# Kernel tuning notes

Measured on AMD Instinct MI355X. Metric: run time of the kernel, lower is better.

Reference implementation:

```python
import jax, jax.numpy as jnp
import numpy as np

N_FEATURE = 12
SIGMA = 0.015
NODES = jnp.linspace(0.0, 0.3, 12)  # RBF centers, matches torch.linspace(0,0.3,12)

B, N, K, FIN = 16, 4096, 32, 4


def setup_inputs() -> dict:
    key = jax.random.key(0)
    ks = jax.random.split(key, 24)

    def make_d(ki, kd):
        idx = jax.random.randint(ki, (B, N, K), 0, N).astype(jnp.float32)
        dist = jax.random.uniform(kd, (B, N, K), minval=0.0, maxval=0.3)
        return jnp.stack([idx, dist], axis=-1)  # [B,N,K,2]

    def lin(kw, kb, fin, fout):
        W = jax.random.normal(kw, (fin, fout), jnp.float32) * (1.0 / np.sqrt(fin))
        b = jax.random.normal(kb, (fout,), jnp.float32) * 0.01
        return W, b

    x = jax.random.normal(ks[0], (B, N, FIN), jnp.float32)
    d1 = make_d(ks[1], ks[2])
    d0 = make_d(ks[3], ks[4])
    dm1 = make_d(ks[5], ks[6])
    mask = jnp.ones((B, N), dtype=bool)

    We, be = lin(ks[7], ks[8], FIN, N_FEATURE)
    Wm1, bm1 = lin(ks[9], ks[10], N_FEATURE + 12, N_FEATURE)
    Wu1, bu1 = lin(ks[11], ks[12], 2 * N_FEATURE, N_FEATURE)
    Wm0, bm0 = lin(ks[13], ks[14], N_FEATURE + 12, N_FEATURE)
    Wu0, bu0 = lin(ks[15], ks[16], 2 * N_FEATURE, N_FEATURE)
    Wmm1, bmm1 = lin(ks[17], ks[18], N_FEATURE + 12, N_FEATURE)
    Wum1, bum1 = lin(ks[19], ks[20], 2 * N_FEATURE, N_FEATURE)

    return {"x": x, "d1": d1, "d0": d0, "dm1": dm1, "mask": mask,
            "We": We, "be": be, "Wm1": Wm1, "bm1": bm1, "Wu1": Wu1, "bu1": bu1,
            "Wm0": Wm0, "bm0": bm0, "Wu0": Wu0, "bu0": bu0,
            "Wmm1": Wmm1, "bmm1": bmm1, "Wum1": Wum1, "bum1": bum1}


def _branch(h, d, Wm, bm, Wu, bu):
    # d: [B,N,K,2] -> channel 0 neighbor index, channel 1 distance
    idx = d[..., 0].astype(jnp.int32)                     # [B,N,K]
    rbf = jnp.exp(-((d[..., 1][..., None] - NODES) ** 2) / (2.0 * SIGMA ** 2))  # [B,N,K,12]
    hj = jax.vmap(lambda hb, ib: hb[ib])(h, idx)          # gather: [B,N,K,F]
    hd = jnp.concatenate([hj, rbf], axis=-1)              # [B,N,K,F+12]
    m = jax.nn.relu(hd @ Wm + bm).sum(axis=2)             # [B,N,F]
    return jax.nn.sigmoid(jnp.concatenate([h, m], axis=-1) @ Wu + bu)  # [B,N,F]


def reference(x, d1, d0, dm1, mask,
              We, be, Wm1, bm1, Wu1, bu1,
              Wm0, bm0, Wu0, bu0,
              Wmm1, bmm1, Wum1, bum1):
    h = jax.nn.relu(x @ We + be)                          # [B,N,12]
    h1 = _branch(h, d1, Wm1, bm1, Wu1, bu1)
    h0 = _branch(h, d0, Wm0, bm0, Wu0, bu0)
    hm1 = _branch(h, dm1, Wmm1, bmm1, Wum1, bum1)
    return (h1, h0, hm1)
```

## Files before the change

kernel.cpp:

```cpp
#include <hip/hip_runtime.h>
#include <hip/hip_fp16.h>
#include <math.h>

#define BBAT 16
#define NNODE 4096
#define KNB 32
#define NF 12
#define TBL 512
#define NPB 820
#define TMAIN 832

#define LDS_BYTES 110616

__device__ __forceinline__ __half2 u2h(unsigned int u) { __half2 h; __builtin_memcpy(&h, &u, 4); return h; }
__device__ __forceinline__ unsigned int h2u(__half2 h) { unsigned int u; __builtin_memcpy(&u, &h, 4); return u; }
__device__ __forceinline__ float4 ldf4(const float* p) { return *(const float4*)p; }

__global__ __launch_bounds__(256) void prep_kernel(
    const float* __restrict__ x, const float* __restrict__ We, const float* __restrict__ be,
    const float* __restrict__ Wm1, const float* __restrict__ bm1,
    const float* __restrict__ Wm0, const float* __restrict__ bm0,
    const float* __restrict__ Wmm1, const float* __restrict__ bmm1,
    float* __restrict__ h, uint4* __restrict__ gA, uint2* __restrict__ gB)
{
    const int node = blockIdx.x * 256 + threadIdx.x;
    float4 xv = ((const float4*)x)[node];
    float hv[NF];
#pragma unroll
    for (int f = 0; f < NF; f++) {
        float s = be[f];
        s = fmaf(xv.x, We[0 * NF + f], s);
        s = fmaf(xv.y, We[1 * NF + f], s);
        s = fmaf(xv.z, We[2 * NF + f], s);
        s = fmaf(xv.w, We[3 * NF + f], s);
        hv[f] = fmaxf(s, 0.0f);
    }
    float4* hp = (float4*)(h + (size_t)node * NF);
    hp[0] = make_float4(hv[0], hv[1], hv[2], hv[3]);
    hp[1] = make_float4(hv[4], hv[5], hv[6], hv[7]);
    hp[2] = make_float4(hv[8], hv[9], hv[10], hv[11]);

#define DO_G(BR, WM, BM) {                                                     \
        float g[NF];                                                           \
        _Pragma("unroll") for (int c = 0; c < NF; c++) {                       \
            float s = BM[c];                                                   \
            _Pragma("unroll") for (int j = 0; j < NF; j++)                     \
                s = fmaf(hv[j], WM[j * NF + c], s);                            \
            g[c] = s;                                                          \
        }                                                                      \
        uint4 a; uint2 bv;                                                     \
        a.x  = h2u(__floats2half2_rn(g[0],  g[1]));                            \
        a.y  = h2u(__floats2half2_rn(g[2],  g[3]));                            \
        a.z  = h2u(__floats2half2_rn(g[4],  g[5]));                            \
        a.w  = h2u(__floats2half2_rn(g[6],  g[7]));                            \
        bv.x = h2u(__floats2half2_rn(g[8],  g[9]));                            \
        bv.y = h2u(__floats2half2_rn(g[10], g[11]));                           \
        gA[(size_t)(BR) * 65536 + node] = a;                                   \
        gB[(size_t)(BR) * 65536 + node] = bv;                                  \
    }
    DO_G(0, Wm1, bm1)
    DO_G(1, Wm0, bm0)
    DO_G(2, Wmm1, bmm1)
#undef DO_G
}

__global__ __launch_bounds__(256) void table_kernel(
    const float* __restrict__ Wm1, const float* __restrict__ Wm0, const float* __restrict__ Wmm1,
    uint4* __restrict__ tA, uint2* __restrict__ tB)
{
    const int br = blockIdx.x;
    const float* Wm = (br == 0) ? Wm1 : (br == 1) ? Wm0 : Wmm1;
    for (int e = threadIdx.x; e < TBL + 1; e += 256) {
        float dd = (float)e * (0.3f / (float)TBL);
        float rbf[12];
#pragma unroll
        for (int j = 0; j < 12; j++) {
            float t = dd - (0.3f / 11.0f) * (float)j;
            rbf[j] = expf(-2222.2222222222f * t * t);
        }
        float ph[NF];
#pragma unroll
        for (int c = 0; c < NF; c++) {
            float s = 0.0f;
#pragma unroll
            for (int j = 0; j < 12; j++) s = fmaf(rbf[j], Wm[(12 + j) * NF + c], s);
            ph[c] = s;
        }
        uint4 a; uint2 bv;
        a.x  = h2u(__floats2half2_rn(ph[0],  ph[1]));
        a.y  = h2u(__floats2half2_rn(ph[2],  ph[3]));
        a.z  = h2u(__floats2half2_rn(ph[4],  ph[5]));
        a.w  = h2u(__floats2half2_rn(ph[6],  ph[7]));
        bv.x = h2u(__floats2half2_rn(ph[8],  ph[9]));
        bv.y = h2u(__floats2half2_rn(ph[10], ph[11]));
        tA[br * (TBL + 1) + e] = a;
        tB[br * (TBL + 1) + e] = bv;
    }
}

__global__ __launch_bounds__(TMAIN) void main_kernel(
    const float* __restrict__ h,
    const uint4* __restrict__ gA, const uint2* __restrict__ gB,
    const uint4* __restrict__ tA, const uint2* __restrict__ tB,
    const float* __restrict__ d1, const float* __restrict__ d0, const float* __restrict__ dm1,
    const float* __restrict__ Wu1, const float* __restrict__ bu1,
    const float* __restrict__ Wu0, const float* __restrict__ bu0,
    const float* __restrict__ Wum1, const float* __restrict__ bum1,
    float* __restrict__ out)
{
    extern __shared__ char smem[];
    uint4* gAl = (uint4*)smem;
    uint2* gBl = (uint2*)(smem + 65536);
    uint4* tAl = (uint4*)(smem + 98304);
    uint2* tBl = (uint2*)(smem + 106512);

    const int q = blockIdx.x, b = blockIdx.y, br = blockIdx.z;
    const int tid = threadIdx.x;
    const size_t slice = (size_t)(br * BBAT + b) * NNODE;

    {
        const uint4* gAg = gA + slice;
        const uint2* gBg = gB + slice;
        for (int i = tid; i < NNODE; i += TMAIN) { gAl[i] = gAg[i]; gBl[i] = gBg[i]; }
        const uint4* tAg = tA + br * (TBL + 1);
        const uint2* tBg = tB + br * (TBL + 1);
        for (int i = tid; i < TBL + 1; i += TMAIN) { tAl[i] = tAg[i]; tBl[i] = tBg[i]; }
    }
    __syncthreads();

    const int n = q * NPB + tid;
    if (tid >= NPB || n >= NNODE) return;

    const float* dsel = (br == 0) ? d1 : (br == 1) ? d0 : dm1;
    const float* Wu   = (br == 0) ? Wu1 : (br == 1) ? Wu0 : Wum1;
    const float* bu   = (br == 0) ? bu1 : (br == 1) ? bu0 : bum1;

    float m[NF];
#pragma unroll
    for (int f = 0; f < NF; f++) m[f] = 0.0f;

    const float4* dp = (const float4*)(dsel + ((size_t)b * NNODE + n) * (size_t)(KNB * 2));

#define ACC(O, G, T0, T1) {                                                    \
        __half2 t0 = u2h(T0), t1 = u2h(T1);                                    \
        __half2 phi = __hfma2(f2, __hsub2(t1, t0), t0);                        \
        __half2 s2 = __hadd2(u2h(G), phi);                                     \
        float2 sf = __half22float2(s2);                                        \
        m[O]     += fmaxf(sf.x, 0.0f);                                         \
        m[O + 1] += fmaxf(sf.y, 0.0f);                                         \
    }

#pragma unroll
    for (int kt = 0; kt < 4; kt++) {
        float4 e0 = dp[kt * 4 + 0];
        float4 e1 = dp[kt * 4 + 1];
        float4 e2 = dp[kt * 4 + 2];
        float4 e3 = dp[kt * 4 + 3];
        float idxf[8] = { e0.x, e0.z, e1.x, e1.z, e2.x, e2.z, e3.x, e3.z };
        float dist[8] = { e0.y, e0.w, e1.y, e1.w, e2.y, e2.w, e3.y, e3.w };
#pragma unroll
        for (int ee = 0; ee < 8; ee++) {
            int j = (int)idxf[ee];
            uint4 ga = gAl[j];
            uint2 gb = gBl[j];
            float uu = dist[ee] * ((float)TBL / 0.3f);
            int i = (int)uu;
            i = min(i, TBL - 1);
            float fr = uu - (float)i;
            __half2 f2 = __float2half2_rn(fr);
            uint4 a0 = tAl[i];
            uint2 b0 = tBl[i];
            uint4 a1 = tAl[i + 1];
            uint2 b1 = tBl[i + 1];
            ACC(0,  ga.x, a0.x, a1.x)
            ACC(2,  ga.y, a0.y, a1.y)
            ACC(4,  ga.z, a0.z, a1.z)
            ACC(6,  ga.w, a0.w, a1.w)
            ACC(8,  gb.x, b0.x, b1.x)
            ACC(10, gb.y, b0.y, b1.y)
        }
    }
#undef ACC

    const float* hp = h + ((size_t)b * NNODE + n) * NF;
    float4 h0 = ldf4(hp), h1v = ldf4(hp + 4), h2v = ldf4(hp + 8);
    float hv[NF] = { h0.x, h0.y, h0.z, h0.w, h1v.x, h1v.y, h1v.z, h1v.w,
                     h2v.x, h2v.y, h2v.z, h2v.w };
    float ov[NF];
#pragma unroll
    for (int f = 0; f < NF; f++) {
        float a = bu[f];
#pragma unroll
        for (int j = 0; j < NF; j++) a = fmaf(hv[j], Wu[j * NF + f], a);
#pragma unroll
        for (int j = 0; j < NF; j++) a = fmaf(m[j], Wu[(NF + j) * NF + f], a);
        ov[f] = 1.0f / (1.0f + __expf(-a));
    }
    float* op = out + (slice + n) * NF;
    ((float4*)op)[0] = make_float4(ov[0], ov[1], ov[2],  ov[3]);
    ((float4*)op)[1] = make_float4(ov[4], ov[5], ov[6],  ov[7]);
    ((float4*)op)[2] = make_float4(ov[8], ov[9], ov[10], ov[11]);
}

extern "C" void kernel_launch(void* const* d_in, const int* in_sizes, int n_in,
                              void* d_out, int out_size, void* d_ws, size_t ws_size,
                              hipStream_t stream)
{
    const float* x    = (const float*)d_in[0];
    const float* d1   = (const float*)d_in[1];
    const float* d0   = (const float*)d_in[2];
    const float* dm1  = (const float*)d_in[3];
    const float* We   = (const float*)d_in[5];
    const float* be   = (const float*)d_in[6];
    const float* Wm1  = (const float*)d_in[7];
    const float* bm1  = (const float*)d_in[8];
    const float* Wu1  = (const float*)d_in[9];
    const float* bu1  = (const float*)d_in[10];
    const float* Wm0  = (const float*)d_in[11];
    const float* bm0  = (const float*)d_in[12];
    const float* Wu0  = (const float*)d_in[13];
    const float* bu0  = (const float*)d_in[14];
    const float* Wmm1 = (const float*)d_in[15];
    const float* bmm1 = (const float*)d_in[16];
    const float* Wum1 = (const float*)d_in[17];
    const float* bum1 = (const float*)d_in[18];

    char* ws = (char*)d_ws;
    float* h  = (float*)ws;
    uint4* gA = (uint4*)(ws + 3145728);
    uint2* gB = (uint2*)(ws + 6291456);
    uint4* tA = (uint4*)(ws + 7864320);
    uint2* tB = (uint2*)(ws + 7888944);

    hipFuncSetAttribute((const void*)main_kernel,
                        hipFuncAttributeMaxDynamicSharedMemorySize, LDS_BYTES);

    prep_kernel<<<dim3(256), 256, 0, stream>>>(
        x, We, be, Wm1, bm1, Wm0, bm0, Wmm1, bmm1, h, gA, gB);
    table_kernel<<<dim3(3), 256, 0, stream>>>(Wm1, Wm0, Wmm1, tA, tB);
    main_kernel<<<dim3(5, BBAT, 3), TMAIN, LDS_BYTES, stream>>>(
        h, gA, gB, tA, tB, d1, d0, dm1,
        Wu1, bu1, Wu0, bu0, Wum1, bum1, (float*)d_out);
}
```

Before: 149.0 us.

## Fuse prep and table kernels into main kernel, computing gathers and table in LDS

```diff
diff --git a/kernel.cpp b/kernel.cpp
--- a/kernel.cpp
+++ b/kernel.cpp
@@ -16,92 +16,11 @@
 __device__ __forceinline__ unsigned int h2u(__half2 h) { unsigned int u; __builtin_memcpy(&u, &h, 4); return u; }
 __device__ __forceinline__ float4 ldf4(const float* p) { return *(const float4*)p; }
 
-__global__ __launch_bounds__(256) void prep_kernel(
+__global__ __launch_bounds__(TMAIN) void fused_kernel(
     const float* __restrict__ x, const float* __restrict__ We, const float* __restrict__ be,
     const float* __restrict__ Wm1, const float* __restrict__ bm1,
     const float* __restrict__ Wm0, const float* __restrict__ bm0,
     const float* __restrict__ Wmm1, const float* __restrict__ bmm1,
-    float* __restrict__ h, uint4* __restrict__ gA, uint2* __restrict__ gB)
-{
-    const int node = blockIdx.x * 256 + threadIdx.x;
-    float4 xv = ((const float4*)x)[node];
-    float hv[NF];
-#pragma unroll
-    for (int f = 0; f < NF; f++) {
-        float s = be[f];
-        s = fmaf(xv.x, We[0 * NF + f], s);
-        s = fmaf(xv.y, We[1 * NF + f], s);
-        s = fmaf(xv.z, We[2 * NF + f], s);
-        s = fmaf(xv.w, We[3 * NF + f], s);
-        hv[f] = fmaxf(s, 0.0f);
-    }
-    float4* hp = (float4*)(h + (size_t)node * NF);
-    hp[0] = make_float4(hv[0], hv[1], hv[2], hv[3]);
-    hp[1] = make_float4(hv[4], hv[5], hv[6], hv[7]);
-    hp[2] = make_float4(hv[8], hv[9], hv[10], hv[11]);
-
-#define DO_G(BR, WM, BM) {                                                     \
-        float g[NF];                                                           \
-        _Pragma("unroll") for (int c = 0; c < NF; c++) {                       \
-            float s = BM[c];                                                   \
-            _Pragma("unroll") for (int j = 0; j < NF; j++)                     \
-                s = fmaf(hv[j], WM[j * NF + c], s);                            \
-            g[c] = s;                                                          \
-        }                                                                      \
-        uint4 a; uint2 bv;                                                     \
-        a.x  = h2u(__floats2half2_rn(g[0],  g[1]));                            \
-        a.y  = h2u(__floats2half2_rn(g[2],  g[3]));                            \
-        a.z  = h2u(__floats2half2_rn(g[4],  g[5]));                            \
-        a.w  = h2u(__floats2half2_rn(g[6],  g[7]));                            \
-        bv.x = h2u(__floats2half2_rn(g[8],  g[9]));                            \
-        bv.y = h2u(__floats2half2_rn(g[10], g[11]));                           \
-        gA[(size_t)(BR) * 65536 + node] = a;                                   \
-        gB[(size_t)(BR) * 65536 + node] = bv;                                  \
-    }
-    DO_G(0, Wm1, bm1)
-    DO_G(1, Wm0, bm0)
-    DO_G(2, Wmm1, bmm1)
-#undef DO_G
-}
-
-__global__ __launch_bounds__(256) void table_kernel(
-    const float* __restrict__ Wm1, const float* __restrict__ Wm0, const float* __restrict__ Wmm1,
-    uint4* __restrict__ tA, uint2* __restrict__ tB)
-{
-    const int br = blockIdx.x;
-    const float* Wm = (br == 0) ? Wm1 : (br == 1) ? Wm0 : Wmm1;
-    for (int e = threadIdx.x; e < TBL + 1; e += 256) {
-        float dd = (float)e * (0.3f / (float)TBL);
-        float rbf[12];
-#pragma unroll
-        for (int j = 0; j < 12; j++) {
-            float t = dd - (0.3f / 11.0f) * (float)j;
-            rbf[j] = expf(-2222.2222222222f * t * t);
-        }
-        float ph[NF];
-#pragma unroll
-        for (int c = 0; c < NF; c++) {
-            float s = 0.0f;
-#pragma unroll
-            for (int j = 0; j < 12; j++) s = fmaf(rbf[j], Wm[(12 + j) * NF + c], s);
-            ph[c] = s;
-        }
-        uint4 a; uint2 bv;
-        a.x  = h2u(__floats2half2_rn(ph[0],  ph[1]));
-        a.y  = h2u(__floats2half2_rn(ph[2],  ph[3]));
-        a.z  = h2u(__floats2half2_rn(ph[4],  ph[5]));
-        a.w  = h2u(__floats2half2_rn(ph[6],  ph[7]));
-        bv.x = h2u(__floats2half2_rn(ph[8],  ph[9]));
-        bv.y = h2u(__floats2half2_rn(ph[10], ph[11]));
-        tA[br * (TBL + 1) + e] = a;
-        tB[br * (TBL + 1) + e] = bv;
-    }
-}
-
-__global__ __launch_bounds__(TMAIN) void main_kernel(
-    const float* __restrict__ h,
-    const uint4* __restrict__ gA, const uint2* __restrict__ gB,
-    const uint4* __restrict__ tA, const uint2* __restrict__ tB,
     const float* __restrict__ d1, const float* __restrict__ d0, const float* __restrict__ dm1,
     const float* __restrict__ Wu1, const float* __restrict__ bu1,
     const float* __restrict__ Wu0, const float* __restrict__ bu0,
@@ -118,13 +37,65 @@
     const int tid = threadIdx.x;
     const size_t slice = (size_t)(br * BBAT + b) * NNODE;
 
-    {
-        const uint4* gAg = gA + slice;
-        const uint2* gBg = gB + slice;
-        for (int i = tid; i < NNODE; i += TMAIN) { gAl[i] = gAg[i]; gBl[i] = gBg[i]; }
-        const uint4* tAg = tA + br * (TBL + 1);
-        const uint2* tBg = tB + br * (TBL + 1);
-        for (int i = tid; i < TBL + 1; i += TMAIN) { tAl[i] = tAg[i]; tBl[i] = tBg[i]; }
+    const float* Wm = (br == 0) ? Wm1 : (br == 1) ? Wm0 : Wmm1;
+    const float* bm = (br == 0) ? bm1 : (br == 1) ? bm0 : bmm1;
+
+    if (tid <= TBL) {
+        float dd = (float)tid * (0.3f / (float)TBL);
+        float rbf[12];
+#pragma unroll
+        for (int j = 0; j < 12; j++) {
+            float t = dd - (0.3f / 11.0f) * (float)j;
+            rbf[j] = expf(-2222.2222222222f * t * t);
+        }
+        float ph[NF];
+#pragma unroll
+        for (int c = 0; c < NF; c++) {
+            float s = 0.0f;
+#pragma unroll
+            for (int j = 0; j < 12; j++) s = fmaf(rbf[j], Wm[(12 + j) * NF + c], s);
+            ph[c] = s;
+        }
+        uint4 a; uint2 bv;
+        a.x  = h2u(__floats2half2_rn(ph[0],  ph[1]));
+        a.y  = h2u(__floats2half2_rn(ph[2],  ph[3]));
+        a.z  = h2u(__floats2half2_rn(ph[4],  ph[5]));
+        a.w  = h2u(__floats2half2_rn(ph[6],  ph[7]));
+        bv.x = h2u(__floats2half2_rn(ph[8],  ph[9]));
+        bv.y = h2u(__floats2half2_rn(ph[10], ph[11]));
+        tAl[tid] = a;
+        tBl[tid] = bv;
+    }
+
+    for (int i = tid; i < NNODE; i += TMAIN) {
+        float4 xv = ((const float4*)x)[(size_t)b * NNODE + i];
+        float hv[NF];
+#pragma unroll
+        for (int f = 0; f < NF; f++) {
+            float s = be[f];
+            s = fmaf(xv.x, We[0 * NF + f], s);
+            s = fmaf(xv.y, We[1 * NF + f], s);
+            s = fmaf(xv.z, We[2 * NF + f], s);
+            s = fmaf(xv.w, We[3 * NF + f], s);
+            hv[f] = fmaxf(s, 0.0f);
+        }
+        float g[NF];
+#pragma unroll
+        for (int c = 0; c < NF; c++) {
+            float s = bm[c];
+#pragma unroll
+            for (int j = 0; j < NF; j++) s = fmaf(hv[j], Wm[j * NF + c], s);
+            g[c] = s;
+        }
+        uint4 a; uint2 bv;
+        a.x  = h2u(__floats2half2_rn(g[0],  g[1]));
+        a.y  = h2u(__floats2half2_rn(g[2],  g[3]));
+        a.z  = h2u(__floats2half2_rn(g[4],  g[5]));
+        a.w  = h2u(__floats2half2_rn(g[6],  g[7]));
+        bv.x = h2u(__floats2half2_rn(g[8],  g[9]));
+        bv.y = h2u(__floats2half2_rn(g[10], g[11]));
+        gAl[i] = a;
+        gBl[i] = bv;
     }
     __syncthreads();
 
@@ -182,10 +153,18 @@
     }
 #undef ACC
 
-    const float* hp = h + ((size_t)b * NNODE + n) * NF;
-    float4 h0 = ldf4(hp), h1v = ldf4(hp + 4), h2v = ldf4(hp + 8);
-    float hv[NF] = { h0.x, h0.y, h0.z, h0.w, h1v.x, h1v.y, h1v.z, h1v.w,
-                     h2v.x, h2v.y, h2v.z, h2v.w };
+    float4 xv = ((const float4*)x)[(size_t)b * NNODE + n];
+    float hv[NF];
+#pragma unroll
+    for (int f = 0; f < NF; f++) {
+        float s = be[f];
+        s = fmaf(xv.x, We[0 * NF + f], s);
+        s = fmaf(xv.y, We[1 * NF + f], s);
+        s = fmaf(xv.z, We[2 * NF + f], s);
+        s = fmaf(xv.w, We[3 * NF + f], s);
+        hv[f] = fmaxf(s, 0.0f);
+    }
+
     float ov[NF];
 #pragma unroll
     for (int f = 0; f < NF; f++) {
@@ -225,20 +204,10 @@
     const float* Wum1 = (const float*)d_in[17];
     const float* bum1 = (const float*)d_in[18];
 
-    char* ws = (char*)d_ws;
-    float* h  = (float*)ws;
-    uint4* gA = (uint4*)(ws + 3145728);
-    uint2* gB = (uint2*)(ws + 6291456);
-    uint4* tA = (uint4*)(ws + 7864320);
-    uint2* tB = (uint2*)(ws + 7888944);
-
-    hipFuncSetAttribute((const void*)main_kernel,
+    hipFuncSetAttribute((const void*)fused_kernel,
                         hipFuncAttributeMaxDynamicSharedMemorySize, LDS_BYTES);
 
-    prep_kernel<<<dim3(256), 256, 0, stream>>>(
-        x, We, be, Wm1, bm1, Wm0, bm0, Wmm1, bmm1, h, gA, gB);
-    table_kernel<<<dim3(3), 256, 0, stream>>>(Wm1, Wm0, Wmm1, tA, tB);
-    main_kernel<<<dim3(5, BBAT, 3), TMAIN, LDS_BYTES, stream>>>(
-        h, gA, gB, tA, tB, d1, d0, dm1,
-        Wu1, bu1, Wu0, bu0, Wum1, bum1, (float*)d_out);
+    fused_kernel<<<dim3(5, BBAT, 3), TMAIN, LDS_BYTES, stream>>>(
+        x, We, be, Wm1, bm1, Wm0, bm0, Wmm1, bmm1,
+        d1, d0, dm1, Wu1, bu1, Wu0, bu0, Wum1, bum1, (float*)d_out);
 }
```

Result: no change. 150.9 us (+1.3%).

## Restructure main kernel: global gathers, two threads per node, XCD-aware block mapping

Applied to the files above, without the earlier changes.

```diff
diff --git a/kernel.cpp b/kernel.cpp
--- a/kernel.cpp
+++ b/kernel.cpp
@@ -7,21 +7,46 @@
 #define KNB 32
 #define NF 12
 #define TBL 512
-#define NPB 820
-#define TMAIN 832
-
-#define LDS_BYTES 110616
+#define TMAIN 512
+#define NPB 256
 
 __device__ __forceinline__ __half2 u2h(unsigned int u) { __half2 h; __builtin_memcpy(&h, &u, 4); return h; }
 __device__ __forceinline__ unsigned int h2u(__half2 h) { unsigned int u; __builtin_memcpy(&u, &h, 4); return u; }
-__device__ __forceinline__ float4 ldf4(const float* p) { return *(const float4*)p; }
+
+__device__ __forceinline__ void phi_entry(int e, const float* __restrict__ Wm, float* ph)
+{
+    float dd = (float)e * (0.3f / (float)TBL);
+    float rbf[12];
+#pragma unroll
+    for (int j = 0; j < 12; j++) {
+        float t = dd - (0.3f / 11.0f) * (float)j;
+        rbf[j] = expf(-2222.2222222222f * t * t);
+    }
+#pragma unroll
+    for (int c = 0; c < NF; c++) {
+        float s = 0.0f;
+#pragma unroll
+        for (int j = 0; j < 12; j++) s = fmaf(rbf[j], Wm[(12 + j) * NF + c], s);
+        ph[c] = s;
+    }
+}
+
+__device__ __forceinline__ void pack12(const float* v, uint4& a, uint2& bv)
+{
+    a.x  = h2u(__floats2half2_rn(v[0],  v[1]));
+    a.y  = h2u(__floats2half2_rn(v[2],  v[3]));
+    a.z  = h2u(__floats2half2_rn(v[4],  v[5]));
+    a.w  = h2u(__floats2half2_rn(v[6],  v[7]));
+    bv.x = h2u(__floats2half2_rn(v[8],  v[9]));
+    bv.y = h2u(__floats2half2_rn(v[10], v[11]));
+}
 
 __global__ __launch_bounds__(256) void prep_kernel(
     const float* __restrict__ x, const float* __restrict__ We, const float* __restrict__ be,
     const float* __restrict__ Wm1, const float* __restrict__ bm1,
     const float* __restrict__ Wm0, const float* __restrict__ bm0,
     const float* __restrict__ Wmm1, const float* __restrict__ bmm1,
-    float* __restrict__ h, uint4* __restrict__ gA, uint2* __restrict__ gB)
+    uint4* __restrict__ gA, uint2* __restrict__ gB, uint4* __restrict__ tP)
 {
     const int node = blockIdx.x * 256 + threadIdx.x;
     float4 xv = ((const float4*)x)[node];
@@ -35,10 +60,6 @@
         s = fmaf(xv.w, We[3 * NF + f], s);
         hv[f] = fmaxf(s, 0.0f);
     }
-    float4* hp = (float4*)(h + (size_t)node * NF);
-    hp[0] = make_float4(hv[0], hv[1], hv[2], hv[3]);
-    hp[1] = make_float4(hv[4], hv[5], hv[6], hv[7]);
-    hp[2] = make_float4(hv[8], hv[9], hv[10], hv[11]);
 
 #define DO_G(BR, WM, BM) {                                                     \
         float g[NF];                                                           \
@@ -49,12 +70,7 @@
             g[c] = s;                                                          \
         }                                                                      \
         uint4 a; uint2 bv;                                                     \
-        a.x  = h2u(__floats2half2_rn(g[0],  g[1]));                            \
-        a.y  = h2u(__floats2half2_rn(g[2],  g[3]));                            \
-        a.z  = h2u(__floats2half2_rn(g[4],  g[5]));                            \
-        a.w  = h2u(__floats2half2_rn(g[6],  g[7]));                            \
-        bv.x = h2u(__floats2half2_rn(g[8],  g[9]));                            \
-        bv.y = h2u(__floats2half2_rn(g[10], g[11]));                           \
+        pack12(g, a, bv);                                                      \
         gA[(size_t)(BR) * 65536 + node] = a;                                   \
         gB[(size_t)(BR) * 65536 + node] = bv;                                  \
     }
@@ -62,84 +78,68 @@
     DO_G(1, Wm0, bm0)
     DO_G(2, Wmm1, bmm1)
 #undef DO_G
-}
-
-__global__ __launch_bounds__(256) void table_kernel(
-    const float* __restrict__ Wm1, const float* __restrict__ Wm0, const float* __restrict__ Wmm1,
-    uint4* __restrict__ tA, uint2* __restrict__ tB)
-{
-    const int br = blockIdx.x;
-    const float* Wm = (br == 0) ? Wm1 : (br == 1) ? Wm0 : Wmm1;
-    for (int e = threadIdx.x; e < TBL + 1; e += 256) {
-        float dd = (float)e * (0.3f / (float)TBL);
-        float rbf[12];
-#pragma unroll
-        for (int j = 0; j < 12; j++) {
-            float t = dd - (0.3f / 11.0f) * (float)j;
-            rbf[j] = expf(-2222.2222222222f * t * t);
+
+    if (blockIdx.x < 3) {
+        const int br = blockIdx.x;
+        const float* Wm = (br == 0) ? Wm1 : (br == 1) ? Wm0 : Wmm1;
+        for (int i = threadIdx.x; i < TBL; i += 256) {
+            float p0[NF], p1[NF];
+            phi_entry(i, Wm, p0);
+            phi_entry(i + 1, Wm, p1);
+            uint4 a0, a1; uint2 b0, b1;
+            pack12(p0, a0, b0);
+            pack12(p1, a1, b1);
+            uint4 w0 = make_uint4(a0.x, a0.y, a0.z, a0.w);
+            uint4 w1 = make_uint4(b0.x, b0.y, a1.x, a1.y);
+            uint4 w2 = make_uint4(a1.z, a1.w, b1.x, b1.y);
+            uint4* dst = tP + ((size_t)br * TBL + i) * 3;
+            dst[0] = w0; dst[1] = w1; dst[2] = w2;
         }
-        float ph[NF];
-#pragma unroll
-        for (int c = 0; c < NF; c++) {
-            float s = 0.0f;
-#pragma unroll
-            for (int j = 0; j < 12; j++) s = fmaf(rbf[j], Wm[(12 + j) * NF + c], s);
-            ph[c] = s;
-        }
-        uint4 a; uint2 bv;
-        a.x  = h2u(__floats2half2_rn(ph[0],  ph[1]));
-        a.y  = h2u(__floats2half2_rn(ph[2],  ph[3]));
-        a.z  = h2u(__floats2half2_rn(ph[4],  ph[5]));
-        a.w  = h2u(__floats2half2_rn(ph[6],  ph[7]));
-        bv.x = h2u(__floats2half2_rn(ph[8],  ph[9]));
-        bv.y = h2u(__floats2half2_rn(ph[10], ph[11]));
-        tA[br * (TBL + 1) + e] = a;
-        tB[br * (TBL + 1) + e] = bv;
-    }
-}
-
-__global__ __launch_bounds__(TMAIN) void main_kernel(
-    const float* __restrict__ h,
-    const uint4* __restrict__ gA, const uint2* __restrict__ gB,
-    const uint4* __restrict__ tA, const uint2* __restrict__ tB,
+    }
+}
+
+__global__ __launch_bounds__(TMAIN, 6) void main_kernel(
+    const float* __restrict__ x, const float* __restrict__ We, const float* __restrict__ be,
+    const uint4* __restrict__ gA, const uint2* __restrict__ gB, const uint4* __restrict__ tP,
     const float* __restrict__ d1, const float* __restrict__ d0, const float* __restrict__ dm1,
     const float* __restrict__ Wu1, const float* __restrict__ bu1,
     const float* __restrict__ Wu0, const float* __restrict__ bu0,
     const float* __restrict__ Wum1, const float* __restrict__ bum1,
     float* __restrict__ out)
 {
-    extern __shared__ char smem[];
-    uint4* gAl = (uint4*)smem;
-    uint2* gBl = (uint2*)(smem + 65536);
-    uint4* tAl = (uint4*)(smem + 98304);
-    uint2* tBl = (uint2*)(smem + 106512);
-
-    const int q = blockIdx.x, b = blockIdx.y, br = blockIdx.z;
+    __shared__ uint4 tPl[TBL * 3];
+
+    const int w = blockIdx.x;
+    const int xcd = w & 7;
+    const int k = w >> 3;
+    const int slice = xcd + 8 * (k >> 4);
+    const int chunk = k & 15;
+    const int br = slice / BBAT;
+    const int b  = slice % BBAT;
+
     const int tid = threadIdx.x;
-    const size_t slice = (size_t)(br * BBAT + b) * NNODE;
 
     {
-        const uint4* gAg = gA + slice;
-        const uint2* gBg = gB + slice;
-        for (int i = tid; i < NNODE; i += TMAIN) { gAl[i] = gAg[i]; gBl[i] = gBg[i]; }
-        const uint4* tAg = tA + br * (TBL + 1);
-        const uint2* tBg = tB + br * (TBL + 1);
-        for (int i = tid; i < TBL + 1; i += TMAIN) { tAl[i] = tAg[i]; tBl[i] = tBg[i]; }
+        const uint4* tPg = tP + (size_t)br * TBL * 3;
+        for (int i = tid; i < TBL * 3; i += TMAIN) tPl[i] = tPg[i];
     }
     __syncthreads();
 
-    const int n = q * NPB + tid;
-    if (tid >= NPB || n >= NNODE) return;
+    const int nl = tid >> 1, half = tid & 1;
+    const int n = chunk * NPB + nl;
 
     const float* dsel = (br == 0) ? d1 : (br == 1) ? d0 : dm1;
     const float* Wu   = (br == 0) ? Wu1 : (br == 1) ? Wu0 : Wum1;
     const float* bu   = (br == 0) ? bu1 : (br == 1) ? bu0 : bum1;
 
+    const uint4* gAg = gA + (size_t)slice * NNODE;
+    const uint2* gBg = gB + (size_t)slice * NNODE;
+
     float m[NF];
 #pragma unroll
     for (int f = 0; f < NF; f++) m[f] = 0.0f;
 
-    const float4* dp = (const float4*)(dsel + ((size_t)b * NNODE + n) * (size_t)(KNB * 2));
+    const float4* dp = (const float4*)(dsel + ((size_t)b * NNODE + n) * (size_t)(KNB * 2)) + half * 8;
 
 #define ACC(O, G, T0, T1) {                                                    \
         __half2 t0 = u2h(T0), t1 = u2h(T1);                                    \
@@ -151,7 +151,7 @@
     }
 
 #pragma unroll
-    for (int kt = 0; kt < 4; kt++) {
+    for (int kt = 0; kt < 2; kt++) {
         float4 e0 = dp[kt * 4 + 0];
         float4 e1 = dp[kt * 4 + 1];
         float4 e2 = dp[kt * 4 + 2];
@@ -161,45 +161,58 @@
 #pragma unroll
         for (int ee = 0; ee < 8; ee++) {
             int j = (int)idxf[ee];
-            uint4 ga = gAl[j];
-            uint2 gb = gBl[j];
+            uint4 ga = gAg[j];
+            uint2 gb = gBg[j];
             float uu = dist[ee] * ((float)TBL / 0.3f);
             int i = (int)uu;
             i = min(i, TBL - 1);
             float fr = uu - (float)i;
             __half2 f2 = __float2half2_rn(fr);
-            uint4 a0 = tAl[i];
-            uint2 b0 = tBl[i];
-            uint4 a1 = tAl[i + 1];
-            uint2 b1 = tBl[i + 1];
-            ACC(0,  ga.x, a0.x, a1.x)
-            ACC(2,  ga.y, a0.y, a1.y)
-            ACC(4,  ga.z, a0.z, a1.z)
-            ACC(6,  ga.w, a0.w, a1.w)
-            ACC(8,  gb.x, b0.x, b1.x)
-            ACC(10, gb.y, b0.y, b1.y)
+            const uint4* tp = &tPl[i * 3];
+            uint4 r0 = tp[0];
+            uint4 r1 = tp[1];
+            uint4 r2 = tp[2];
+            ACC(0,  ga.x, r0.x, r1.z)
+            ACC(2,  ga.y, r0.y, r1.w)
+            ACC(4,  ga.z, r0.z, r2.x)
+            ACC(6,  ga.w, r0.w, r2.y)
+            ACC(8,  gb.x, r1.x, r2.z)
+            ACC(10, gb.y, r1.y, r2.w)
         }
     }
 #undef ACC
 
-    const float* hp = h + ((size_t)b * NNODE + n) * NF;
-    float4 h0 = ldf4(hp), h1v = ldf4(hp + 4), h2v = ldf4(hp + 8);
-    float hv[NF] = { h0.x, h0.y, h0.z, h0.w, h1v.x, h1v.y, h1v.z, h1v.w,
-                     h2v.x, h2v.y, h2v.z, h2v.w };
-    float ov[NF];
+#pragma unroll
+    for (int f = 0; f < NF; f++) m[f] += __shfl_xor(m[f], 1);
+
+    float4 xv = ((const float4*)x)[(size_t)b * NNODE + n];
+    float hv[NF];
 #pragma unroll
     for (int f = 0; f < NF; f++) {
+        float s = be[f];
+        s = fmaf(xv.x, We[0 * NF + f], s);
+        s = fmaf(xv.y, We[1 * NF + f], s);
+        s = fmaf(xv.z, We[2 * NF + f], s);
+        s = fmaf(xv.w, We[3 * NF + f], s);
+        hv[f] = fmaxf(s, 0.0f);
+    }
+
+    const int f0 = half * 6;
+    float ov[6];
+#pragma unroll
+    for (int ff = 0; ff < 6; ff++) {
+        const int f = f0 + ff;
         float a = bu[f];
 #pragma unroll
         for (int j = 0; j < NF; j++) a = fmaf(hv[j], Wu[j * NF + f], a);
 #pragma unroll
         for (int j = 0; j < NF; j++) a = fmaf(m[j], Wu[(NF + j) * NF + f], a);
-        ov[f] = 1.0f / (1.0f + __expf(-a));
-    }
-    float* op = out + (slice + n) * NF;
-    ((float4*)op)[0] = make_float4(ov[0], ov[1], ov[2],  ov[3]);
-    ((float4*)op)[1] = make_float4(ov[4], ov[5], ov[6],  ov[7]);
-    ((float4*)op)[2] = make_float4(ov[8], ov[9], ov[10], ov[11]);
+        ov[ff] = 1.0f / (1.0f + __expf(-a));
+    }
+    float* op = out + ((size_t)slice * NNODE + n) * NF + f0;
+    ((float2*)op)[0] = make_float2(ov[0], ov[1]);
+    ((float2*)op)[1] = make_float2(ov[2], ov[3]);
+    ((float2*)op)[2] = make_float2(ov[4], ov[5]);
 }
 
 extern "C" void kernel_launch(void* const* d_in, const int* in_sizes, int n_in,
@@ -226,19 +239,13 @@
     const float* bum1 = (const float*)d_in[18];
 
     char* ws = (char*)d_ws;
-    float* h  = (float*)ws;
-    uint4* gA = (uint4*)(ws + 3145728);
-    uint2* gB = (uint2*)(ws + 6291456);
-    uint4* tA = (uint4*)(ws + 7864320);
-    uint2* tB = (uint2*)(ws + 7888944);
-
-    hipFuncSetAttribute((const void*)main_kernel,
-                        hipFuncAttributeMaxDynamicSharedMemorySize, LDS_BYTES);
+    uint4* gA = (uint4*)ws;
+    uint2* gB = (uint2*)(ws + 3145728);
+    uint4* tP = (uint4*)(ws + 4718592);
 
     prep_kernel<<<dim3(256), 256, 0, stream>>>(
-        x, We, be, Wm1, bm1, Wm0, bm0, Wmm1, bmm1, h, gA, gB);
-    table_kernel<<<dim3(3), 256, 0, stream>>>(Wm1, Wm0, Wmm1, tA, tB);
-    main_kernel<<<dim3(5, BBAT, 3), TMAIN, LDS_BYTES, stream>>>(
-        h, gA, gB, tA, tB, d1, d0, dm1,
+        x, We, be, Wm1, bm1, Wm0, bm0, Wmm1, bmm1, gA, gB, tP);
+    main_kernel<<<dim3(768), TMAIN, 0, stream>>>(
+        x, We, be, gA, gB, tP, d1, d0, dm1,
         Wu1, bu1, Wu0, bu0, Wum1, bum1, (float*)d_out);
 }
```

Measured after the change: 180.2 us. 1.21x slower.
